# Kernel optimization log

Hardware: AMD Instinct MI355X
Metric: run time of the kernel (lower is better)

The kernel has to match this reference:

```python
import jax, jax.numpy as jnp
import numpy as np

HID = 512; NH = 8; FEAT = 128; NCELLS = 64; NGRAPHS = 64; NODES_PER = 64; DEG = 16
SCALE = 0.02


def setup_inputs() -> dict:
    key = jax.random.key(0)
    ks = iter(jax.random.split(key, 32))
    counts_np = 2 + (np.arange(NCELLS) % 7)              # genes per cell, 2..8
    G = int(counts_np.sum())                              # 317 total genes
    cell_ids_np = np.repeat(np.arange(NCELLS), counts_np)
    rank_np = np.concatenate([np.arange(c) for c in counts_np])
    Lmax = int(counts_np.max()) * NGRAPHS                 # padded per-cell seq len
    N = NGRAPHS * NODES_PER
    E = N * DEG
    rn = lambda k, s: jax.random.normal(k, s, dtype=jnp.float32) * SCALE
    inp = {
        'x': jax.random.normal(next(ks), (N, FEAT), dtype=jnp.float32),
        'edge_index': jax.random.randint(next(ks), (2, E), 0, N, dtype=jnp.int32),
        'batch': jnp.repeat(jnp.arange(NGRAPHS, dtype=jnp.int32), NODES_PER),
        'gene_W': rn(next(ks), (G, FEAT, HID)),
        'gene_b': jnp.zeros((G, HID), jnp.float32),
        'cell_ids': jnp.asarray(cell_ids_np, jnp.int32),
        'rank': jnp.asarray(rank_np, jnp.int32),
        'counts': jnp.asarray(counts_np, jnp.int32),
        'Wq': rn(next(ks), (HID, HID)), 'bq': jnp.zeros((HID,), jnp.float32),
        'Wk': rn(next(ks), (HID, HID)), 'bk': jnp.zeros((HID,), jnp.float32),
        'Wv': rn(next(ks), (HID, HID)), 'bv': jnp.zeros((HID,), jnp.float32),
        'Wo': rn(next(ks), (HID, HID)), 'bo': jnp.zeros((HID,), jnp.float32),
        'Wi1': rn(next(ks), (HID, 2 * HID)), 'bi1': jnp.zeros((2 * HID,), jnp.float32),
        'Wi2': rn(next(ks), (2 * HID, HID)), 'bi2': jnp.zeros((HID,), jnp.float32),
        'ln_g': jnp.ones((HID,), jnp.float32), 'ln_b': jnp.zeros((HID,), jnp.float32),
        'Aw1': rn(next(ks), (NCELLS, HID, HID)), 'Ab1': jnp.zeros((NCELLS, HID), jnp.float32),
        'Aw2': rn(next(ks), (NCELLS, HID)), 'Ab2': jnp.zeros((NCELLS,), jnp.float32),
        'Lmax': Lmax,
        'num_graphs': NGRAPHS,
    }
    return inp


def reference(x, edge_index, batch, gene_W, gene_b, cell_ids, rank, counts,
              Wq, bq, Wk, bk, Wv, bv, Wo, bo,
              Wi1, bi1, Wi2, bi2, ln_g, ln_b,
              Aw1, Ab1, Aw2, Ab2, Lmax, num_graphs):
    N = x.shape[0]; H = Wq.shape[0]; nh = NH; dh = H // nh
    C = counts.shape[0]; B = num_graphs
    # --- gene GNN: one-hop mean aggregation + per-graph mean pool + per-gene Linear/ReLU ---
    src, dst = edge_index[0], edge_index[1]
    deg = jax.ops.segment_sum(jnp.ones((src.shape[0],), x.dtype), dst, num_segments=N)
    agg = jax.ops.segment_sum(x[src], dst, num_segments=N)
    xn = x + agg / jnp.maximum(deg, 1.0)[:, None]
    gsum = jax.ops.segment_sum(xn, batch, num_segments=B)
    gcnt = jax.ops.segment_sum(jnp.ones((N,), x.dtype), batch, num_segments=B)
    pooled = gsum / gcnt[:, None]                                  # [B, F]
    gene_out = jax.nn.relu(jnp.einsum('bf,gfh->gbh', pooled, gene_W) + gene_b[:, None, :])  # [G,B,H]
    # --- ragged regroup: rows of gene g go to cell cell_ids[g] at positions rank[g]*B + b ---
    pos = rank[:, None] * B + jnp.arange(B)[None, :]               # [G, B]
    padded = jnp.zeros((C, Lmax, H), x.dtype).at[cell_ids[:, None], pos].set(gene_out)
    seqlen = counts * B                                            # valid length per cell
    valid = jnp.arange(Lmax)[None, :] < seqlen[:, None]            # [C, Lmax]
    # --- shared multi-head self-attention over each cell's gene rows (key padding mask) ---
    q = (padded @ Wq + bq).reshape(C, Lmax, nh, dh)
    k = (padded @ Wk + bk).reshape(C, Lmax, nh, dh)
    v = (padded @ Wv + bv).reshape(C, Lmax, nh, dh)
    scores = jnp.einsum('clhd,cmhd->chlm', q, k) * (1.0 / np.sqrt(dh))
    scores = jnp.where(valid[:, None, None, :], scores, -1e9)
    attn = jax.nn.softmax(scores, axis=-1)
    attended = jnp.einsum('chlm,cmhd->clhd', attn, v).reshape(C, Lmax, H) @ Wo + bo
    vf = valid.astype(x.dtype)
    meanh = (attended * vf[:, :, None]).sum(axis=1) / seqlen[:, None].astype(x.dtype)  # [C,H]
    # --- shared integrator: Linear -> ReLU -> (Dropout=eval identity) -> Linear -> LayerNorm ---
    h = jax.nn.relu(meanh @ Wi1 + bi1) @ Wi2 + bi2
    mu = h.mean(-1, keepdims=True)
    var = ((h - mu) ** 2).mean(-1, keepdims=True)
    integrated = (h - mu) / jnp.sqrt(var + 1e-5) * ln_g + ln_b     # [C, H]
    # --- per-cell affinity heads ---
    h1 = jax.nn.relu(jnp.einsum('ch,chk->ck', integrated, Aw1) + Ab1)
    aff = jax.nn.sigmoid(jnp.einsum('ck,ck->c', h1, Aw2) + Ab2)
    return aff[:, None], integrated[:, None, :]
```

## Files before the change

### kernel.cpp

```cpp
#include <hip/hip_runtime.h>
#include <hip/hip_bf16.h>
#include <math.h>

#define NNODES 4096
#define NEDGES 65536
#define NFEAT  128
#define NPG    64
#define NG     317
#define NB     64
#define H      512
#define DH     64
#define NROWS  20288
#define MPAD   20352

typedef __attribute__((ext_vector_type(8))) short short8v;
typedef __attribute__((ext_vector_type(4))) float float4v;

#define WS_DEG    0u
#define WS_AGG    4096u
#define WS_POOLED 528384u
#define WS_ROWSB  536576u
#define WS_WT     5730304u
#define WS_QB     6123520u
#define WS_KB     11333632u
#define WS_VB     16543744u
#define WS_CTX    21753856u
#define WS_HAFF   21786624u
#define WS_MEANH  21819392u
#define WS_TMP1   21852160u
#define WS_INTEG  21917696u

__device__ __forceinline__ float bf2f(ushort u) {
    union { unsigned int i; float f; } x; x.i = ((unsigned int)u) << 16; return x.f;
}

__global__ void deg_kernel(const int* __restrict__ ei, float* __restrict__ deg) {
    int e = blockIdx.x * 256 + threadIdx.x;
    atomicAdd(&deg[ei[NEDGES + e]], 1.0f);
}

__global__ void agg_kernel(const int* __restrict__ ei, const float* __restrict__ x,
                           float* __restrict__ agg) {
    int idx = blockIdx.x * 256 + threadIdx.x;
    int e = idx >> 5, f4 = idx & 31;
    int s = ei[e], d = ei[NEDGES + e];
    float4 v = ((const float4*)x)[s * 32 + f4];
    float* a = &agg[d * NFEAT + f4 * 4];
    atomicAdd(a + 0, v.x);
    atomicAdd(a + 1, v.y);
    atomicAdd(a + 2, v.z);
    atomicAdd(a + 3, v.w);
}

__global__ void pooled_kernel(const float* __restrict__ x, const float* __restrict__ agg,
                              const float* __restrict__ deg, float* __restrict__ pooled) {
    int b = blockIdx.x, f = threadIdx.x;
    float s = 0.f;
    for (int i = 0; i < NPG; ++i) {
        int n = b * NPG + i;
        s += x[n * NFEAT + f] + agg[n * NFEAT + f] / fmaxf(deg[n], 1.0f);
    }
    pooled[b * NFEAT + f] = s * (1.0f / 64.0f);
}

__global__ __launch_bounds__(256) void gene_kernel(const float* __restrict__ pooled,
        const float* __restrict__ gW, const float* __restrict__ gb, ushort* __restrict__ rowsb) {
    __shared__ float ps[NB * NFEAT];
    int g = blockIdx.x, t = threadIdx.x;
    int h = blockIdx.y * 256 + t;
    for (int i = t; i < NB * NFEAT; i += 256) ps[i] = pooled[i];
    __syncthreads();
    float acc[NB];
    #pragma unroll
    for (int b = 0; b < NB; ++b) acc[b] = 0.f;
    const float* wp = &gW[(size_t)g * NFEAT * H + h];
    for (int f4 = 0; f4 < NFEAT; f4 += 4) {
        float w0 = wp[(f4 + 0) * H], w1 = wp[(f4 + 1) * H];
        float w2 = wp[(f4 + 2) * H], w3 = wp[(f4 + 3) * H];
        #pragma unroll
        for (int b = 0; b < NB; ++b) {
            float4 p = *(const float4*)&ps[b * NFEAT + f4];
            acc[b] += p.x * w0 + p.y * w1 + p.z * w2 + p.w * w3;
        }
    }
    float bias = gb[g * H + h];
    #pragma unroll
    for (int b = 0; b < NB; ++b) {
        float val = fmaxf(acc[b] + bias, 0.f);
        __hip_bfloat16 bv = __float2bfloat16(val);
        rowsb[(size_t)(g * NB + b) * H + h] = *(ushort*)&bv;
    }
}

__global__ void wcvt_kernel(const float* __restrict__ Wq, const float* __restrict__ Wk,
                            const float* __restrict__ Wv, ushort* __restrict__ WT) {
    __shared__ float tile[32][33];
    int z = blockIdx.z;
    const float* W = z == 0 ? Wq : (z == 1 ? Wk : Wv);
    ushort* out = WT + (size_t)z * H * H;
    int k0 = blockIdx.x * 32, n0 = blockIdx.y * 32;
    int tx = threadIdx.x, ty = threadIdx.y;
    for (int j = 0; j < 32; j += 8)
        tile[ty + j][tx] = W[(size_t)(k0 + ty + j) * H + n0 + tx];
    __syncthreads();
    for (int j = 0; j < 32; j += 8) {
        __hip_bfloat16 b = __float2bfloat16(tile[tx][ty + j]);
        out[(size_t)(n0 + ty + j) * H + k0 + tx] = *(ushort*)&b;
    }
}

__global__ __launch_bounds__(256) void qkv_mfma(const ushort* __restrict__ rowsb,
        const ushort* __restrict__ WT,
        const float* __restrict__ bq, const float* __restrict__ bk, const float* __restrict__ bv,
        ushort* __restrict__ q, ushort* __restrict__ k, ushort* __restrict__ v) {
    __shared__ ushort As[128][68];
    __shared__ ushort Bs[128][68];
    int nt = blockIdx.x, mt = blockIdx.y;
    int m0 = mt * 128;
    int n0g = nt * 128;
    int z = n0g >> 9;
    int n0 = n0g & 511;
    const float* bias = z == 0 ? bq : (z == 1 ? bk : bv);
    ushort* out = z == 0 ? q : (z == 1 ? k : v);
    int t = threadIdx.x;
    int wave = t >> 6, lane = t & 63;
    int wr = wave >> 1, wc = wave & 1;
    int fr = lane & 15, fq = lane >> 4;
    int srow = t >> 1, shalf = t & 1;
    int grow = m0 + srow; grow = grow < NROWS ? grow : NROWS - 1;
    const ushort* gaBase = &rowsb[(size_t)grow * H + shalf * 32];
    const ushort* gbBase = &WT[(size_t)(n0g + srow) * H + shalf * 32];
    float4v acc[4][4] = {};
    uint4 ar[4], br[4];
    #pragma unroll
    for (int i = 0; i < 4; ++i) {
        ar[i] = *(const uint4*)(gaBase + i * 8);
        br[i] = *(const uint4*)(gbBase + i * 8);
    }
    for (int kt = 0; kt < 8; ++kt) {
        __syncthreads();
        #pragma unroll
        for (int i = 0; i < 4; ++i) {
            *(uint4*)&As[srow][shalf * 32 + i * 8] = ar[i];
            *(uint4*)&Bs[srow][shalf * 32 + i * 8] = br[i];
        }
        __syncthreads();
        if (kt < 7) {
            int k0n = (kt + 1) * 64;
            #pragma unroll
            for (int i = 0; i < 4; ++i) {
                ar[i] = *(const uint4*)(gaBase + k0n + i * 8);
                br[i] = *(const uint4*)(gbBase + k0n + i * 8);
            }
        }
        #pragma unroll
        for (int s2 = 0; s2 < 2; ++s2) {
            short8v af[4], bf[4];
            #pragma unroll
            for (int mi = 0; mi < 4; ++mi)
                af[mi] = *(const short8v*)&As[wr * 64 + mi * 16 + fr][s2 * 32 + fq * 8];
            #pragma unroll
            for (int ni = 0; ni < 4; ++ni)
                bf[ni] = *(const short8v*)&Bs[wc * 64 + ni * 16 + fr][s2 * 32 + fq * 8];
            #pragma unroll
            for (int mi = 0; mi < 4; ++mi)
                #pragma unroll
                for (int ni = 0; ni < 4; ++ni)
                    acc[mi][ni] = __builtin_amdgcn_mfma_f32_16x16x32_bf16(af[mi], bf[ni], acc[mi][ni], 0, 0, 0);
        }
    }
    float bcol[4];
    #pragma unroll
    for (int ni = 0; ni < 4; ++ni) bcol[ni] = bias[n0 + wc * 64 + ni * 16 + fr];
    #pragma unroll
    for (int mi = 0; mi < 4; ++mi) {
        #pragma unroll
        for (int rr = 0; rr < 4; ++rr) {
            size_t rbase = (size_t)(m0 + wr * 64 + mi * 16 + fq * 4 + rr) * H;
            #pragma unroll
            for (int ni = 0; ni < 4; ++ni) {
                int col = n0 + wc * 64 + ni * 16 + fr;
                __hip_bfloat16 b = __float2bfloat16(acc[mi][ni][rr] + bcol[ni]);
                out[rbase + col] = *(ushort*)&b;
            }
        }
    }
}

__global__ __launch_bounds__(64) void attn_kernel(const ushort* __restrict__ q,
        const ushort* __restrict__ k, const ushort* __restrict__ v,
        const int* __restrict__ counts, float* __restrict__ ctx) {
    __shared__ float w_lds[64];
    int qt = blockIdx.x, h = blockIdx.y, c = blockIdx.z;
    int cnt = counts[c];
    if (qt * 32 >= cnt * 64) return;
    int cs = 0;
    for (int i = 0; i < c; ++i) cs += counts[i];
    int lane = threadIdx.x;
    int fr = lane & 15, fkb = (lane >> 4) * 8;
    size_t rowbase = (size_t)(cs * 64) * H + (size_t)h * DH;
    const ushort* qp = q + rowbase + (size_t)(qt * 32) * H;
    const ushort* kp = k + rowbase;
    const ushort* vp = v + rowbase;
    short8v qf[2][2];
    #pragma unroll
    for (int mi = 0; mi < 2; ++mi)
        #pragma unroll
        for (int s = 0; s < 2; ++s)
            qf[mi][s] = *(const short8v*)&qp[(size_t)(mi * 16 + fr) * H + s * 32 + fkb];
    float4v dacc[2] = {};
    for (int kt = 0; kt < cnt; ++kt) {
        const ushort* kpt = kp + (size_t)(kt * 64) * H;
        short8v kf[4][2];
        #pragma unroll
        for (int n = 0; n < 4; ++n)
            #pragma unroll
            for (int s = 0; s < 2; ++s)
                kf[n][s] = *(const short8v*)&kpt[(size_t)(n * 16 + fr) * H + s * 32 + fkb];
        #pragma unroll
        for (int mi = 0; mi < 2; ++mi) {
            #pragma unroll
            for (int n = 0; n < 4; ++n) {
                float4v acc = {};
                acc = __builtin_amdgcn_mfma_f32_16x16x32_bf16(qf[mi][0], kf[n][0], acc, 0, 0, 0);
                acc = __builtin_amdgcn_mfma_f32_16x16x32_bf16(qf[mi][1], kf[n][1], acc, 0, 0, 0);
                #pragma unroll
                for (int rr = 0; rr < 4; ++rr)
                    dacc[mi][rr] += __expf(acc[rr] * 0.125f);
            }
        }
    }
    #pragma unroll
    for (int off = 1; off < 16; off <<= 1) {
        #pragma unroll
        for (int mi = 0; mi < 2; ++mi)
            #pragma unroll
            for (int rr = 0; rr < 4; ++rr)
                dacc[mi][rr] += __shfl_xor(dacc[mi][rr], off, 64);
    }
    float4v invd[2];
    #pragma unroll
    for (int mi = 0; mi < 2; ++mi)
        #pragma unroll
        for (int rr = 0; rr < 4; ++rr)
            invd[mi][rr] = 1.0f / dacc[mi][rr];
    float o0 = 0.f, o1 = 0.f, o2 = 0.f, o3 = 0.f;
    for (int kt = 0; kt < cnt; ++kt) {
        const ushort* kpt = kp + (size_t)(kt * 64) * H;
        short8v kf[4][2];
        #pragma unroll
        for (int n = 0; n < 4; ++n)
            #pragma unroll
            for (int s = 0; s < 2; ++s)
                kf[n][s] = *(const short8v*)&kpt[(size_t)(n * 16 + fr) * H + s * 32 + fkb];
        float wpart[4] = {0.f, 0.f, 0.f, 0.f};
        #pragma unroll
        for (int mi = 0; mi < 2; ++mi) {
            #pragma unroll
            for (int n = 0; n < 4; ++n) {
                float4v acc = {};
                acc = __builtin_amdgcn_mfma_f32_16x16x32_bf16(qf[mi][0], kf[n][0], acc, 0, 0, 0);
                acc = __builtin_amdgcn_mfma_f32_16x16x32_bf16(qf[mi][1], kf[n][1], acc, 0, 0, 0);
                #pragma unroll
                for (int rr = 0; rr < 4; ++rr)
                    wpart[n] += __expf(acc[rr] * 0.125f) * invd[mi][rr];
            }
        }
        #pragma unroll
        for (int n = 0; n < 4; ++n) {
            wpart[n] += __shfl_xor(wpart[n], 16, 64);
            wpart[n] += __shfl_xor(wpart[n], 32, 64);
        }
        if (lane < 16) {
            #pragma unroll
            for (int n = 0; n < 4; ++n) w_lds[n * 16 + lane] = wpart[n];
        }
        __syncthreads();
        const ushort* vrow = vp + (size_t)(kt * 64) * H;
        #pragma unroll 4
        for (int key = 0; key < 64; key += 4) {
            float w0 = w_lds[key + 0], w1 = w_lds[key + 1];
            float w2 = w_lds[key + 2], w3 = w_lds[key + 3];
            o0 += w0 * bf2f(vrow[(size_t)(key + 0) * H + lane]);
            o1 += w1 * bf2f(vrow[(size_t)(key + 1) * H + lane]);
            o2 += w2 * bf2f(vrow[(size_t)(key + 2) * H + lane]);
            o3 += w3 * bf2f(vrow[(size_t)(key + 3) * H + lane]);
        }
        __syncthreads();
    }
    atomicAdd(&ctx[c * H + h * DH + lane], (o0 + o1) + (o2 + o3));
}

__global__ __launch_bounds__(512) void meanh_kernel(const float* __restrict__ ctx,
        const float* __restrict__ Wo, const float* __restrict__ bo,
        const int* __restrict__ counts, float* __restrict__ meanh) {
    __shared__ float cs[H];
    int c = blockIdx.x, j = threadIdx.x;
    cs[j] = ctx[c * H + j];
    __syncthreads();
    float acc = 0.f;
    for (int i = 0; i < H; ++i) acc += cs[i] * Wo[i * H + j];
    meanh[c * H + j] = acc / (float)(counts[c] * 64) + bo[j];
}

__global__ __launch_bounds__(1024) void ff1_kernel(const float* __restrict__ meanh,
        const float* __restrict__ Wi1, const float* __restrict__ bi1, float* __restrict__ tmp1) {
    __shared__ float ms[H];
    int c = blockIdx.x, j = threadIdx.x;
    if (j < H) ms[j] = meanh[c * H + j];
    __syncthreads();
    float acc = 0.f;
    for (int i = 0; i < H; ++i) acc += ms[i] * Wi1[i * 1024 + j];
    tmp1[c * 1024 + j] = fmaxf(acc + bi1[j], 0.f);
}

__device__ __forceinline__ float block_sum512(float val, float* red8) {
    #pragma unroll
    for (int off = 32; off; off >>= 1) val += __shfl_xor(val, off, 64);
    int w = threadIdx.x >> 6;
    if ((threadIdx.x & 63) == 0) red8[w] = val;
    __syncthreads();
    float s = red8[0] + red8[1] + red8[2] + red8[3] + red8[4] + red8[5] + red8[6] + red8[7];
    __syncthreads();
    return s;
}

__global__ __launch_bounds__(512) void ln_kernel(const float* __restrict__ tmp1,
        const float* __restrict__ Wi2, const float* __restrict__ bi2,
        const float* __restrict__ ln_g, const float* __restrict__ ln_b,
        float* __restrict__ integ_out, float* __restrict__ out) {
    __shared__ float t1[1024];
    __shared__ float red8[8];
    int c = blockIdx.x, j = threadIdx.x;
    t1[j] = tmp1[c * 1024 + j];
    t1[j + 512] = tmp1[c * 1024 + j + 512];
    __syncthreads();
    float acc = 0.f;
    for (int i = 0; i < 1024; ++i) acc += t1[i] * Wi2[i * H + j];
    float hval = acc + bi2[j];
    float mu = block_sum512(hval, red8) * (1.0f / 512.0f);
    float d = hval - mu;
    float var = block_sum512(d * d, red8) * (1.0f / 512.0f);
    float integ = d * rsqrtf(var + 1e-5f) * ln_g[j] + ln_b[j];
    out[64 + c * H + j] = integ;
    integ_out[c * H + j] = integ;
}

__global__ __launch_bounds__(512) void affin1_kernel(const float* __restrict__ integ,
        const float* __restrict__ Aw1, float* __restrict__ haff) {
    __shared__ float is[128];
    int c = blockIdx.x, sl = blockIdx.y, j = threadIdx.x;
    if (j < 128) is[j] = integ[c * H + sl * 128 + j];
    __syncthreads();
    const float* A1 = Aw1 + (size_t)c * H * H + (size_t)sl * 128 * H;
    float acc = 0.f;
    for (int i = 0; i < 128; ++i) acc += is[i] * A1[i * H + j];
    atomicAdd(&haff[c * H + j], acc);
}

__global__ __launch_bounds__(512) void affin2_kernel(const float* __restrict__ haff,
        const float* __restrict__ Ab1, const float* __restrict__ Aw2,
        const float* __restrict__ Ab2, float* __restrict__ out) {
    __shared__ float red8[8];
    int c = blockIdx.x, j = threadIdx.x;
    float h1 = fmaxf(haff[c * H + j] + Ab1[c * H + j], 0.f);
    float part = h1 * Aw2[c * H + j];
    float tot = block_sum512(part, red8);
    if (j == 0) out[c] = 1.0f / (1.0f + __expf(-(tot + Ab2[c])));
}

extern "C" void kernel_launch(void* const* d_in, const int* in_sizes, int n_in,
                              void* d_out, int out_size, void* d_ws, size_t ws_size,
                              hipStream_t stream) {
    const float* x      = (const float*)d_in[0];
    const int*   ei     = (const int*)d_in[1];
    const float* gene_W = (const float*)d_in[3];
    const float* gene_b = (const float*)d_in[4];
    const int*   counts = (const int*)d_in[7];
    const float* Wq = (const float*)d_in[8];  const float* bq = (const float*)d_in[9];
    const float* Wk = (const float*)d_in[10]; const float* bk = (const float*)d_in[11];
    const float* Wv = (const float*)d_in[12]; const float* bv = (const float*)d_in[13];
    const float* Wo = (const float*)d_in[14]; const float* bo = (const float*)d_in[15];
    const float* Wi1 = (const float*)d_in[16]; const float* bi1 = (const float*)d_in[17];
    const float* Wi2 = (const float*)d_in[18]; const float* bi2 = (const float*)d_in[19];
    const float* ln_g = (const float*)d_in[20]; const float* ln_b = (const float*)d_in[21];
    const float* Aw1 = (const float*)d_in[22]; const float* Ab1 = (const float*)d_in[23];
    const float* Aw2 = (const float*)d_in[24]; const float* Ab2 = (const float*)d_in[25];
    float* ws = (float*)d_ws;
    float* outp = (float*)d_out;
    ushort* rowsb = (ushort*)(ws + WS_ROWSB);
    ushort* WT    = (ushort*)(ws + WS_WT);
    ushort* qb    = (ushort*)(ws + WS_QB);
    ushort* kb    = (ushort*)(ws + WS_KB);
    ushort* vb    = (ushort*)(ws + WS_VB);

    hipMemsetAsync(ws + WS_DEG, 0, (size_t)WS_POOLED * sizeof(float), stream);
    hipMemsetAsync(ws + WS_CTX, 0, (size_t)65536 * sizeof(float), stream);

    deg_kernel<<<NEDGES / 256, 256, 0, stream>>>(ei, ws + WS_DEG);
    agg_kernel<<<NEDGES * 32 / 256, 256, 0, stream>>>(ei, x, ws + WS_AGG);
    pooled_kernel<<<NB, NFEAT, 0, stream>>>(x, ws + WS_AGG, ws + WS_DEG, ws + WS_POOLED);
    gene_kernel<<<dim3(NG, 2), 256, 0, stream>>>(ws + WS_POOLED, gene_W, gene_b, rowsb);
    wcvt_kernel<<<dim3(16, 16, 3), dim3(32, 8), 0, stream>>>(Wq, Wk, Wv, WT);
    qkv_mfma<<<dim3(12, 159), 256, 0, stream>>>(rowsb, WT, bq, bk, bv, qb, kb, vb);
    attn_kernel<<<dim3(16, 8, 64), 64, 0, stream>>>(qb, kb, vb, counts, ws + WS_CTX);
    meanh_kernel<<<NB, H, 0, stream>>>(ws + WS_CTX, Wo, bo, counts, ws + WS_MEANH);
    ff1_kernel<<<NB, 1024, 0, stream>>>(ws + WS_MEANH, Wi1, bi1, ws + WS_TMP1);
    ln_kernel<<<NB, H, 0, stream>>>(ws + WS_TMP1, Wi2, bi2, ln_g, ln_b,
        ws + WS_INTEG, outp);
    affin1_kernel<<<dim3(NB, 4), H, 0, stream>>>(ws + WS_INTEG, Aw1, ws + WS_HAFF);
    affin2_kernel<<<NB, H, 0, stream>>>(ws + WS_HAFF, Ab1, Aw2, Ab2, outp);
}
```

Baseline: 798.9 us.

## Fuse deg into agg, fuse meanh+ff1, XCD-remap and LDS-staged stores in qkv GEMM

The degree count moves into the aggregation kernel, so one launch disappears. The meanh and ff1 kernels merge into a single 1024-thread kernel. The QKV MFMA GEMM now runs on a 1D grid whose tile indices are remapped so each XCD gets a contiguous range of tiles, which is meant to improve L2 reuse. Its bf16 output is staged through a shared LDS buffer so global stores are coalesced 16-byte writes instead of scattered 2-byte ones, at the cost of an extra barrier and LDS traffic.

```diff
diff --git a/kernel.cpp b/kernel.cpp
--- a/kernel.cpp
+++ b/kernel.cpp
@@ -34,16 +34,12 @@
     union { unsigned int i; float f; } x; x.i = ((unsigned int)u) << 16; return x.f;
 }
 
-__global__ void deg_kernel(const int* __restrict__ ei, float* __restrict__ deg) {
-    int e = blockIdx.x * 256 + threadIdx.x;
-    atomicAdd(&deg[ei[NEDGES + e]], 1.0f);
-}
-
 __global__ void agg_kernel(const int* __restrict__ ei, const float* __restrict__ x,
-                           float* __restrict__ agg) {
+                           float* __restrict__ agg, float* __restrict__ deg) {
     int idx = blockIdx.x * 256 + threadIdx.x;
     int e = idx >> 5, f4 = idx & 31;
     int s = ei[e], d = ei[NEDGES + e];
+    if (f4 == 0) atomicAdd(&deg[d], 1.0f);
     float4 v = ((const float4*)x)[s * 32 + f4];
     float* a = &agg[d * NFEAT + f4 * 4];
     atomicAdd(a + 0, v.x);
@@ -113,9 +109,12 @@
         const ushort* __restrict__ WT,
         const float* __restrict__ bq, const float* __restrict__ bk, const float* __restrict__ bv,
         ushort* __restrict__ q, ushort* __restrict__ k, ushort* __restrict__ v) {
-    __shared__ ushort As[128][68];
-    __shared__ ushort Bs[128][68];
-    int nt = blockIdx.x, mt = blockIdx.y;
+    __shared__ ushort smem[18944];
+    int bid = blockIdx.x;
+    int xcd = bid & 7, pos = bid >> 3;
+    int start = xcd < 4 ? xcd * 239 : 4 * 239 + (xcd - 4) * 238;
+    int tid = start + pos;
+    int mt = tid / 12, nt = tid - mt * 12;
     int m0 = mt * 128;
     int n0g = nt * 128;
     int z = n0g >> 9;
@@ -130,6 +129,8 @@
     int grow = m0 + srow; grow = grow < NROWS ? grow : NROWS - 1;
     const ushort* gaBase = &rowsb[(size_t)grow * H + shalf * 32];
     const ushort* gbBase = &WT[(size_t)(n0g + srow) * H + shalf * 32];
+    #define AS(r, c) smem[(r) * 68 + (c)]
+    #define BS(r, c) smem[8704 + (r) * 68 + (c)]
     float4v acc[4][4] = {};
     uint4 ar[4], br[4];
     #pragma unroll
@@ -141,8 +142,8 @@
         __syncthreads();
         #pragma unroll
         for (int i = 0; i < 4; ++i) {
-            *(uint4*)&As[srow][shalf * 32 + i * 8] = ar[i];
-            *(uint4*)&Bs[srow][shalf * 32 + i * 8] = br[i];
+            *(uint4*)&AS(srow, shalf * 32 + i * 8) = ar[i];
+            *(uint4*)&BS(srow, shalf * 32 + i * 8) = br[i];
         }
         __syncthreads();
         if (kt < 7) {
@@ -158,10 +159,10 @@
             short8v af[4], bf[4];
             #pragma unroll
             for (int mi = 0; mi < 4; ++mi)
-                af[mi] = *(const short8v*)&As[wr * 64 + mi * 16 + fr][s2 * 32 + fq * 8];
+                af[mi] = *(const short8v*)&AS(wr * 64 + mi * 16 + fr, s2 * 32 + fq * 8);
             #pragma unroll
             for (int ni = 0; ni < 4; ++ni)
-                bf[ni] = *(const short8v*)&Bs[wc * 64 + ni * 16 + fr][s2 * 32 + fq * 8];
+                bf[ni] = *(const short8v*)&BS(wc * 64 + ni * 16 + fr, s2 * 32 + fq * 8);
             #pragma unroll
             for (int mi = 0; mi < 4; ++mi)
                 #pragma unroll
@@ -172,19 +173,30 @@
     float bcol[4];
     #pragma unroll
     for (int ni = 0; ni < 4; ++ni) bcol[ni] = bias[n0 + wc * 64 + ni * 16 + fr];
+    __syncthreads();
     #pragma unroll
     for (int mi = 0; mi < 4; ++mi) {
         #pragma unroll
         for (int rr = 0; rr < 4; ++rr) {
-            size_t rbase = (size_t)(m0 + wr * 64 + mi * 16 + fq * 4 + rr) * H;
+            int row = wr * 64 + mi * 16 + fq * 4 + rr;
             #pragma unroll
             for (int ni = 0; ni < 4; ++ni) {
-                int col = n0 + wc * 64 + ni * 16 + fr;
+                int col = wc * 64 + ni * 16 + fr;
                 __hip_bfloat16 b = __float2bfloat16(acc[mi][ni][rr] + bcol[ni]);
-                out[rbase + col] = *(ushort*)&b;
+                smem[row * 148 + col] = *(ushort*)&b;
             }
         }
     }
+    __syncthreads();
+    int crow = t >> 4, cseg = t & 15;
+    #pragma unroll
+    for (int p = 0; p < 8; ++p) {
+        int row = p * 16 + crow;
+        uint4 val = *(const uint4*)&smem[row * 148 + cseg * 8];
+        *(uint4*)&out[(size_t)(m0 + row) * H + n0 + cseg * 8] = val;
+    }
+    #undef AS
+    #undef BS
 }
 
 __global__ __launch_bounds__(64) void attn_kernel(const ushort* __restrict__ q,
@@ -291,23 +303,21 @@
     atomicAdd(&ctx[c * H + h * DH + lane], (o0 + o1) + (o2 + o3));
 }
 
-__global__ __launch_bounds__(512) void meanh_kernel(const float* __restrict__ ctx,
+__global__ __launch_bounds__(1024) void meanff1_kernel(const float* __restrict__ ctx,
         const float* __restrict__ Wo, const float* __restrict__ bo,
-        const int* __restrict__ counts, float* __restrict__ meanh) {
+        const int* __restrict__ counts,
+        const float* __restrict__ Wi1, const float* __restrict__ bi1,
+        float* __restrict__ tmp1) {
     __shared__ float cs[H];
-    int c = blockIdx.x, j = threadIdx.x;
-    cs[j] = ctx[c * H + j];
-    __syncthreads();
-    float acc = 0.f;
-    for (int i = 0; i < H; ++i) acc += cs[i] * Wo[i * H + j];
-    meanh[c * H + j] = acc / (float)(counts[c] * 64) + bo[j];
-}
-
-__global__ __launch_bounds__(1024) void ff1_kernel(const float* __restrict__ meanh,
-        const float* __restrict__ Wi1, const float* __restrict__ bi1, float* __restrict__ tmp1) {
     __shared__ float ms[H];
     int c = blockIdx.x, j = threadIdx.x;
-    if (j < H) ms[j] = meanh[c * H + j];
+    if (j < H) cs[j] = ctx[c * H + j];
+    __syncthreads();
+    if (j < H) {
+        float acc = 0.f;
+        for (int i = 0; i < H; ++i) acc += cs[i] * Wo[i * H + j];
+        ms[j] = acc / (float)(counts[c] * 64) + bo[j];
+    }
     __syncthreads();
     float acc = 0.f;
     for (int i = 0; i < H; ++i) acc += ms[i] * Wi1[i * 1024 + j];
@@ -397,15 +407,14 @@
     hipMemsetAsync(ws + WS_DEG, 0, (size_t)WS_POOLED * sizeof(float), stream);
     hipMemsetAsync(ws + WS_CTX, 0, (size_t)65536 * sizeof(float), stream);
 
-    deg_kernel<<<NEDGES / 256, 256, 0, stream>>>(ei, ws + WS_DEG);
-    agg_kernel<<<NEDGES * 32 / 256, 256, 0, stream>>>(ei, x, ws + WS_AGG);
+    agg_kernel<<<NEDGES * 32 / 256, 256, 0, stream>>>(ei, x, ws + WS_AGG, ws + WS_DEG);
     pooled_kernel<<<NB, NFEAT, 0, stream>>>(x, ws + WS_AGG, ws + WS_DEG, ws + WS_POOLED);
     gene_kernel<<<dim3(NG, 2), 256, 0, stream>>>(ws + WS_POOLED, gene_W, gene_b, rowsb);
     wcvt_kernel<<<dim3(16, 16, 3), dim3(32, 8), 0, stream>>>(Wq, Wk, Wv, WT);
-    qkv_mfma<<<dim3(12, 159), 256, 0, stream>>>(rowsb, WT, bq, bk, bv, qb, kb, vb);
+    qkv_mfma<<<1908, 256, 0, stream>>>(rowsb, WT, bq, bk, bv, qb, kb, vb);
     attn_kernel<<<dim3(16, 8, 64), 64, 0, stream>>>(qb, kb, vb, counts, ws + WS_CTX);
-    meanh_kernel<<<NB, H, 0, stream>>>(ws + WS_CTX, Wo, bo, counts, ws + WS_MEANH);
-    ff1_kernel<<<NB, 1024, 0, stream>>>(ws + WS_MEANH, Wi1, bi1, ws + WS_TMP1);
+    meanff1_kernel<<<NB, 1024, 0, stream>>>(ws + WS_CTX, Wo, bo, counts, Wi1, bi1,
+        ws + WS_TMP1);
     ln_kernel<<<NB, H, 0, stream>>>(ws + WS_TMP1, Wi2, bi2, ln_g, ln_b,
         ws + WS_INTEG, outp);
     affin1_kernel<<<dim3(NB, 4), H, 0, stream>>>(ws + WS_INTEG, Aw1, ws + WS_HAFF);
```

Result: no change. 792.0 us (-0.9%).
